# Kernel tuning notes

Hardware: AMD Instinct MI355X
Metric: run time of the kernel (lower is better)

## Reference

```python
import jax, jax.numpy as jnp
import numpy as np

D_MODEL = 1024
N_HEADS = 16
HEAD_DIM = D_MODEL // N_HEADS
BATCH = 2
SEQ = 2048


def setup_inputs() -> dict:
    key = jax.random.key(0)
    ks = jax.random.split(key, 9)
    s = 1.0 / np.sqrt(D_MODEL)
    inp = {
        "x": jax.random.normal(ks[0], (BATCH, SEQ, D_MODEL), dtype=jnp.float32),
        "Wq": jax.random.uniform(ks[1], (D_MODEL, D_MODEL), jnp.float32, -s, s),
        "bq": jax.random.uniform(ks[2], (D_MODEL,), jnp.float32, -s, s),
        "Wk": jax.random.uniform(ks[3], (D_MODEL, D_MODEL), jnp.float32, -s, s),
        "bk": jax.random.uniform(ks[4], (D_MODEL,), jnp.float32, -s, s),
        "Wv": jax.random.uniform(ks[5], (D_MODEL, D_MODEL), jnp.float32, -s, s),
        "bv": jax.random.uniform(ks[6], (D_MODEL,), jnp.float32, -s, s),
        "Wo": jax.random.uniform(ks[7], (D_MODEL, D_MODEL), jnp.float32, -s, s),
        "bo": jax.random.uniform(ks[8], (D_MODEL,), jnp.float32, -s, s),
    }
    return inp


def reference(x, Wq, bq, Wk, bk, Wv, bv, Wo, bo):
    B, S, _ = x.shape
    # projections -> [B, H, S, Dh]
    def proj(W, b):
        y = jnp.einsum('bsd,df->bsf', x, W) + b
        return y.reshape(B, S, N_HEADS, HEAD_DIM).transpose(0, 2, 1, 3)
    q = proj(Wq, bq)
    k = proj(Wk, bk)
    v = proj(Wv, bv)
    scores = jnp.einsum('bhqd,bhkd->bhqk', q, k) / jnp.sqrt(jnp.float32(HEAD_DIM))
    mask = jnp.tril(jnp.ones((S, S), dtype=bool))  # [S, S] causal mask
    scores = jnp.where(mask, scores, -jnp.inf)
    weights = jax.nn.softmax(scores, axis=-1)
    h = jnp.einsum('bhqk,bhkd->bhqd', weights, v)
    h = h.transpose(0, 2, 1, 3).reshape(B, S, N_HEADS * HEAD_DIM)
    return jnp.einsum('bsd,df->bsf', h, Wo) + bo
```

## Files before the change

kernel.cpp:

```cpp
#include <hip/hip_runtime.h>
#include <hip/hip_bf16.h>
#include <cmath>

#define D_MODEL 1024
#define NHEADS 16
#define HDIM 64
#define BATCH 2
#define SEQ 2048
#define MROWS (BATCH*SEQ)
#define KDIM 1024

typedef unsigned short ushort_t;
typedef unsigned int uint32;
typedef __attribute__((ext_vector_type(8))) short short8;
typedef __attribute__((ext_vector_type(4))) short short4b;
typedef __attribute__((ext_vector_type(4))) float floatx4;

#define QSCALE 0.1803368801111204f
#define EXP2F(x) __builtin_amdgcn_exp2f(x)

__device__ __forceinline__ ushort_t f2bf(float x) {
    union { float f; uint32 u; } v; v.f = x;
    uint32 r = v.u + 0x7FFFu + ((v.u >> 16) & 1u);
    return (ushort_t)(r >> 16);
}

__device__ __forceinline__ uint32 pkbf(float a, float b) {
    union { __hip_bfloat162 h2; uint32 u; } v;
    v.h2 = __float22bfloat162_rn(make_float2(a, b));
    return v.u;
}

__device__ __forceinline__ void glds16(const void* g, void* l) {
    __builtin_amdgcn_global_load_lds(
        (const __attribute__((address_space(1))) void*)g,
        (__attribute__((address_space(3))) void*)l, 16, 0, 0);
}

__global__ __launch_bounds__(256)
void cvt_all(const float* __restrict__ x, const float* __restrict__ W0,
             const float* __restrict__ W1, const float* __restrict__ W2,
             const float* __restrict__ W3, ushort_t* __restrict__ xb,
             ushort_t* __restrict__ WtQKV, ushort_t* __restrict__ WtO)
{
    const int z = blockIdx.z;
    if (z == 4) {
        size_t idx = ((size_t)blockIdx.y * 32 + blockIdx.x) * 256 + threadIdx.x;
        #pragma unroll
        for (int l = 0; l < 4; ++l) {
            size_t i = ((size_t)l * 262144 + idx) * 4;
            float4 v = *(const float4*)(x + i);
            uint2 o;
            o.x = pkbf(v.x, v.y);
            o.y = pkbf(v.z, v.w);
            *(uint2*)(xb + i) = o;
        }
        return;
    }
    __shared__ float tl[32][33];
    const float* W = (z == 0) ? W0 : (z == 1) ? W1 : (z == 2) ? W2 : W3;
    ushort_t* out = (z < 3) ? (WtQKV + (size_t)z * D_MODEL * KDIM) : WtO;
    const int k0 = blockIdx.x * 32, n0 = blockIdx.y * 32;
    const int tx = threadIdx.x & 31, ty = threadIdx.x >> 5;
    #pragma unroll
    for (int i = 0; i < 4; ++i)
        tl[ty + i * 8][tx] = W[(size_t)(k0 + ty + i * 8) * D_MODEL + n0 + tx];
    __syncthreads();
    #pragma unroll
    for (int i = 0; i < 4; ++i)
        out[(size_t)(n0 + ty + i * 8) * KDIM + k0 + tx] = f2bf(tl[tx][ty + i * 8]);
}

__global__ __launch_bounds__(128, 2)
void gemm_qkv(const ushort_t* __restrict__ A, const ushort_t* __restrict__ Bt,
              const float* __restrict__ b0, const float* __restrict__ b1,
              const float* __restrict__ b2, ushort_t* __restrict__ Qb,
              ushort_t* __restrict__ Kb, ushort_t* __restrict__ Vb)
{
    __shared__ ushort_t As[128 * 64];
    __shared__ ushort_t Bs[128 * 64];

    const int tid = threadIdx.x;
    const int w = tid >> 6, lane = tid & 63;
    const int quad = lane >> 4, col = lane & 15;
    const int m0 = blockIdx.y * 128, n0 = blockIdx.x * 128;

    floatx4 zero = {0.f, 0.f, 0.f, 0.f};
    floatx4 acc[4][8];
    #pragma unroll
    for (int i = 0; i < 4; ++i)
        #pragma unroll
        for (int j = 0; j < 8; ++j) acc[i][j] = zero;

    #pragma unroll 1
    for (int k0 = 0; k0 < KDIM; k0 += 64) {
        #pragma unroll
        for (int i = 0; i < 8; ++i) {
            int c = i * 128 + tid;
            int row = c >> 3;
            int kc = (c & 7) ^ (row & 7);
            glds16(A  + (size_t)(m0 + row) * KDIM + k0 + kc * 8, As + (i * 128 + w * 64) * 8);
            glds16(Bt + (size_t)(n0 + row) * KDIM + k0 + kc * 8, Bs + (i * 128 + w * 64) * 8);
        }
        __syncthreads();
        #pragma unroll
        for (int ks = 0; ks < 2; ++ks) {
            short8 af[4], bfr[8];
            const int kc = ks * 4 + quad;
            #pragma unroll
            for (int mt = 0; mt < 4; ++mt) {
                int r = w * 64 + mt * 16 + col;
                af[mt] = *(const short8*)(As + ((size_t)r * 8 + (kc ^ (r & 7))) * 8);
            }
            #pragma unroll
            for (int nt = 0; nt < 8; ++nt) {
                int r = nt * 16 + col;
                bfr[nt] = *(const short8*)(Bs + ((size_t)r * 8 + (kc ^ (r & 7))) * 8);
            }
            #pragma unroll
            for (int mt = 0; mt < 4; ++mt)
                #pragma unroll
                for (int nt = 0; nt < 8; ++nt)
                    acc[mt][nt] = __builtin_amdgcn_mfma_f32_16x16x32_bf16(
                        af[mt], bfr[nt], acc[mt][nt], 0, 0, 0);
        }
        __syncthreads();
    }

    const int which = n0 >> 10;
    const float* bp = (which == 0) ? b0 : (which == 1) ? b1 : b2;
    if (which < 2) {
        ushort_t* outp = (which == 0) ? Qb : Kb;
        const float scl = (which == 0) ? QSCALE : 1.0f;
        #pragma unroll
        for (int mt = 0; mt < 4; ++mt)
            #pragma unroll
            for (int nt = 0; nt < 8; ++nt) {
                int nn = (n0 + nt * 16 + col) & 1023;
                float bb = bp[nn];
                int h = nn >> 6, d = nn & 63;
                #pragma unroll
                for (int r = 0; r < 4; ++r) {
                    int m = m0 + w * 64 + mt * 16 + quad * 4 + r;
                    int b = m >> 11, s = m & 2047;
                    outp[((size_t)(b * NHEADS + h) * SEQ + s) * HDIM + d] =
                        f2bf((acc[mt][nt][r] + bb) * scl);
                }
            }
    } else {
        #pragma unroll
        for (int mt = 0; mt < 4; ++mt)
            #pragma unroll
            for (int nt = 0; nt < 8; ++nt) {
                int nn = (n0 + nt * 16 + col) & 1023;
                float bb = bp[nn];
                int h = nn >> 6, d = nn & 63;
                int mb = m0 + w * 64 + mt * 16 + quad * 4;
                int b = mb >> 11, s = mb & 2047;
                uint2 pw;
                pw.x = pkbf(acc[mt][nt][0] + bb, acc[mt][nt][1] + bb);
                pw.y = pkbf(acc[mt][nt][2] + bb, acc[mt][nt][3] + bb);
                *(uint2*)(Vb + ((size_t)(b * NHEADS + h) * HDIM + d) * SEQ + s) = pw;
            }
    }
}

__global__ __launch_bounds__(128, 2)
void gemm_o(const ushort_t* __restrict__ A, const ushort_t* __restrict__ Bt,
            const float* __restrict__ b0, float* __restrict__ Cf)
{
    __shared__ ushort_t As[128 * 64];
    __shared__ ushort_t Bs[64 * 64];

    const int tid = threadIdx.x;
    const int w = tid >> 6, lane = tid & 63;
    const int quad = lane >> 4, col = lane & 15;
    const int m0 = blockIdx.y * 128, n0 = blockIdx.x * 64;

    floatx4 zero = {0.f, 0.f, 0.f, 0.f};
    floatx4 acc[4][4];
    #pragma unroll
    for (int i = 0; i < 4; ++i)
        #pragma unroll
        for (int j = 0; j < 4; ++j) acc[i][j] = zero;

    #pragma unroll 1
    for (int k0 = 0; k0 < KDIM; k0 += 64) {
        #pragma unroll
        for (int i = 0; i < 8; ++i) {
            int c = i * 128 + tid;
            int row = c >> 3;
            int kc = (c & 7) ^ (row & 7);
            glds16(A + (size_t)(m0 + row) * KDIM + k0 + kc * 8, As + (i * 128 + w * 64) * 8);
        }
        #pragma unroll
        for (int i = 0; i < 4; ++i) {
            int c = i * 128 + tid;
            int row = c >> 3;
            int kc = (c & 7) ^ (row & 7);
            glds16(Bt + (size_t)(n0 + row) * KDIM + k0 + kc * 8, Bs + (i * 128 + w * 64) * 8);
        }
        __syncthreads();
        #pragma unroll
        for (int ks = 0; ks < 2; ++ks) {
            short8 af[4], bfr[4];
            const int kc = ks * 4 + quad;
            #pragma unroll
            for (int mt = 0; mt < 4; ++mt) {
                int r = w * 64 + mt * 16 + col;
                af[mt] = *(const short8*)(As + ((size_t)r * 8 + (kc ^ (r & 7))) * 8);
            }
            #pragma unroll
            for (int nt = 0; nt < 4; ++nt) {
                int r = nt * 16 + col;
                bfr[nt] = *(const short8*)(Bs + ((size_t)r * 8 + (kc ^ (r & 7))) * 8);
            }
            #pragma unroll
            for (int mt = 0; mt < 4; ++mt)
                #pragma unroll
                for (int nt = 0; nt < 4; ++nt)
                    acc[mt][nt] = __builtin_amdgcn_mfma_f32_16x16x32_bf16(
                        af[mt], bfr[nt], acc[mt][nt], 0, 0, 0);
        }
        __syncthreads();
    }

    #pragma unroll
    for (int mt = 0; mt < 4; ++mt)
        #pragma unroll
        for (int nt = 0; nt < 4; ++nt) {
            int n = n0 + nt * 16 + col;
            float bb = b0[n];
            #pragma unroll
            for (int r = 0; r < 4; ++r) {
                int m = m0 + w * 64 + mt * 16 + quad * 4 + r;
                Cf[(size_t)m * D_MODEL + n] = acc[mt][nt][r] + bb;
            }
        }
}

__global__ __launch_bounds__(256)
void attn_mfma(const ushort_t* __restrict__ Q, const ushort_t* __restrict__ K,
               const ushort_t* __restrict__ Vt, ushort_t* __restrict__ H)
{
    __shared__ __align__(16) float smemf[16640];
    ushort_t* Qs  = (ushort_t*)smemf;
    ushort_t* Ksm = (ushort_t*)(smemf + 2048);
    ushort_t* Vsm = (ushort_t*)(smemf + 6144);
    float* Ored = smemf;
    float* Lred = smemf + 16384;

    const int tid = threadIdx.x;
    const int w = tid >> 6, lane = tid & 63;
    const int quad = lane >> 4, col = lane & 15;
    const int blk = blockIdx.x;
    const int bh = (blk & 7) * 4 + ((blk >> 3) & 3);
    const int pair = blk >> 5;
    const size_t base = (size_t)bh * SEQ * HDIM;
    const ushort_t* Kb = K + base;
    const ushort_t* Vb = Vt + base;
    const int b = bh >> 4, h = bh & 15;

    const int c0 = (w * 2 + 0) * 64 + lane;
    const int c1 = (w * 2 + 1) * 64 + lane;
    const int r0 = c0 >> 3, o0 = ((c0 & 7) ^ (r0 & 7)) * 8;
    const int r1 = c1 >> 3, o1 = ((c1 & 7) ^ (r1 & 7)) * 8;

    const int rk = w * 16 + col;
    const floatx4 zero = {0.f, 0.f, 0.f, 0.f};

    #pragma unroll 1
    for (int pi = 0; pi < 2; ++pi) {
        const int qt = pi ? pair : 31 - pair;
        const int q0 = qt * 64;
        const int nt = qt + 1;

        __syncthreads();
        #pragma unroll
        for (int i = 0; i < 2; ++i) {
            int c = (w * 2 + i) * 64 + lane;
            int row = c >> 3, kc = (c & 7) ^ (row & 7);
            glds16(Q + base + (size_t)(q0 + row) * HDIM + kc * 8, Qs + (w * 2 + i) * 512);
        }
        glds16(Kb + (size_t)r0 * HDIM + o0, Ksm + (w * 2 + 0) * 512);
        glds16(Kb + (size_t)r1 * HDIM + o1, Ksm + (w * 2 + 1) * 512);
        glds16(Vb + (size_t)r0 * SEQ + o0,  Vsm + (w * 2 + 0) * 512);
        glds16(Vb + (size_t)r1 * SEQ + o1,  Vsm + (w * 2 + 1) * 512);
        __syncthreads();

        short8 bq[4][2];
        #pragma unroll
        for (int qb = 0; qb < 4; ++qb)
            #pragma unroll
            for (int ks = 0; ks < 2; ++ks) {
                int rq = qb * 16 + col;
                int kc = ks * 4 + quad;
                bq[qb][ks] = *(const short8*)(Qs + ((size_t)rq * 8 + (kc ^ (rq & 7))) * 8);
            }

        floatx4 o_[4][4];
        #pragma unroll
        for (int i = 0; i < 4; ++i)
            #pragma unroll
            for (int j = 0; j < 4; ++j) o_[i][j] = zero;
        float lq[4] = {0.f, 0.f, 0.f, 0.f};

        #pragma unroll 1
        for (int t = 0; t < nt; ++t) {
            const ushort_t* Kcur = Ksm + (t & 1) * 4096;
            const ushort_t* Vcur = Vsm + (t & 1) * 4096;
            if (t + 1 < nt) {
                const int k0n = (t + 1) * 64;
                ushort_t* Kn = Ksm + ((t + 1) & 1) * 4096;
                ushort_t* Vn = Vsm + ((t + 1) & 1) * 4096;
                glds16(Kb + (size_t)(k0n + r0) * HDIM + o0, Kn + (w * 2 + 0) * 512);
                glds16(Kb + (size_t)(k0n + r1) * HDIM + o1, Kn + (w * 2 + 1) * 512);
                glds16(Vb + (size_t)r0 * SEQ + k0n + o0,    Vn + (w * 2 + 0) * 512);
                glds16(Vb + (size_t)r1 * SEQ + k0n + o1,    Vn + (w * 2 + 1) * 512);
            }

            floatx4 sc[4];
            #pragma unroll
            for (int qb = 0; qb < 4; ++qb) sc[qb] = zero;
            #pragma unroll
            for (int ks = 0; ks < 2; ++ks) {
                const int kc = ks * 4 + quad;
                short8 ak = *(const short8*)(Kcur + ((size_t)rk * 8 + (kc ^ (rk & 7))) * 8);
                #pragma unroll
                for (int qb = 0; qb < 4; ++qb)
                    sc[qb] = __builtin_amdgcn_mfma_f32_16x16x32_bf16(
                        ak, bq[qb][ks], sc[qb], 0, 0, 0);
            }

            if (t == nt - 1) {
                #pragma unroll
                for (int qb = 0; qb < 4; ++qb)
                    #pragma unroll
                    for (int r = 0; r < 4; ++r)
                        if (w * 16 + quad * 4 + r > qb * 16 + col) sc[qb][r] = -INFINITY;
            }

            short4b bp[4];
            #pragma unroll
            for (int qb = 0; qb < 4; ++qb) {
                float p0 = EXP2F(sc[qb][0]);
                float p1 = EXP2F(sc[qb][1]);
                float p2 = EXP2F(sc[qb][2]);
                float p3 = EXP2F(sc[qb][3]);
                lq[qb] += (p0 + p1) + (p2 + p3);
                union { uint2 u; short4b s; } pv;
                pv.u.x = pkbf(p0, p1);
                pv.u.y = pkbf(p2, p3);
                bp[qb] = pv.s;
            }

            const int cc = 2 * w + (quad >> 1);
            const int sub = (quad & 1) * 4;
            #pragma unroll
            for (int db = 0; db < 4; ++db) {
                int rv = db * 16 + col;
                short4b av = *(const short4b*)(Vcur + ((size_t)rv * 8 + (cc ^ (rv & 7))) * 8 + sub);
                #pragma unroll
                for (int qb = 0; qb < 4; ++qb)
                    o_[db][qb] = __builtin_amdgcn_mfma_f32_16x16x16bf16_1k(
                        av, bp[qb], o_[db][qb], 0, 0, 0);
            }

            __syncthreads();
        }

        #pragma unroll
        for (int qb = 0; qb < 4; ++qb) {
            lq[qb] += __shfl_xor(lq[qb], 16);
            lq[qb] += __shfl_xor(lq[qb], 32);
        }
        if (quad == 0) {
            #pragma unroll
            for (int qb = 0; qb < 4; ++qb) Lred[w * 64 + qb * 16 + col] = lq[qb];
        }
        {
            float* myreg = Ored + w * 4096;
            #pragma unroll
            for (int db = 0; db < 4; ++db)
                #pragma unroll
                for (int qb = 0; qb < 4; ++qb) {
                    int q = qb * 16 + col;
                    int swch = (db * 4 + quad) ^ col;
                    *(floatx4*)(myreg + q * 64 + swch * 4) = o_[db][qb];
                }
        }
        __syncthreads();

        {
            const int qloc = w * 16 + (lane >> 2);
            float lsum = Lred[qloc] + Lred[64 + qloc] + Lred[128 + qloc] + Lred[192 + qloc];
            float linv = 1.f / lsum;
            const int dc0 = (lane & 3) * 4;
            floatx4 acc[4];
            #pragma unroll
            for (int j = 0; j < 4; ++j) {
                int swch = (dc0 + j) ^ (qloc & 15);
                const float* p = Ored + (size_t)qloc * 64 + swch * 4;
                floatx4 a = *(const floatx4*)p;
                a += *(const floatx4*)(p + 4096);
                a += *(const floatx4*)(p + 8192);
                a += *(const floatx4*)(p + 12288);
                acc[j] = a;
            }
            const size_t rowb = ((size_t)(b * SEQ + q0 + qloc)) * D_MODEL + h * HDIM + dc0 * 4;
            uint4 u0, u1;
            u0.x = pkbf(acc[0][0] * linv, acc[0][1] * linv);
            u0.y = pkbf(acc[0][2] * linv, acc[0][3] * linv);
            u0.z = pkbf(acc[1][0] * linv, acc[1][1] * linv);
            u0.w = pkbf(acc[1][2] * linv, acc[1][3] * linv);
            u1.x = pkbf(acc[2][0] * linv, acc[2][1] * linv);
            u1.y = pkbf(acc[2][2] * linv, acc[2][3] * linv);
            u1.z = pkbf(acc[3][0] * linv, acc[3][1] * linv);
            u1.w = pkbf(acc[3][2] * linv, acc[3][3] * linv);
            *(uint4*)(H + rowb) = u0;
            *(uint4*)(H + rowb + 8) = u1;
        }
    }
}

extern "C" void kernel_launch(void* const* d_in, const int* in_sizes, int n_in,
                              void* d_out, int out_size, void* d_ws, size_t ws_size,
                              hipStream_t stream)
{
    (void)in_sizes; (void)n_in; (void)out_size; (void)ws_size;
    const float* x  = (const float*)d_in[0];
    const float* Wq = (const float*)d_in[1];
    const float* bq = (const float*)d_in[2];
    const float* Wk = (const float*)d_in[3];
    const float* bk = (const float*)d_in[4];
    const float* Wv = (const float*)d_in[5];
    const float* bv = (const float*)d_in[6];
    const float* Wo = (const float*)d_in[7];
    const float* bo = (const float*)d_in[8];

    const size_t E = (size_t)MROWS * D_MODEL;
    ushort_t* xb    = (ushort_t*)d_ws;
    ushort_t* WtQKV = xb + E;
    ushort_t* WtO   = WtQKV + 3 * (size_t)D_MODEL * KDIM;
    ushort_t* Qb    = WtO + (size_t)D_MODEL * KDIM;
    ushort_t* Kb    = Qb + E;
    ushort_t* Vb    = Kb + E;
    ushort_t* Hb    = Vb + E;

    cvt_all<<<dim3(32, 32, 5), 256, 0, stream>>>(x, Wq, Wk, Wv, Wo, xb, WtQKV, WtO);
    gemm_qkv<<<dim3(24, 32), 128, 0, stream>>>(xb, WtQKV, bq, bk, bv, Qb, Kb, Vb);
    attn_mfma<<<dim3(512), 256, 0, stream>>>(Qb, Kb, Vb, Hb);
    gemm_o<<<dim3(16, 32), 128, 0, stream>>>(Hb, WtO, bo, (float*)d_out);
}
```

Measured before the change: 179.2 us.

## Fuse conversion, QKV GEMM, attention and output GEMM into one persistent kernel

New measurement: 389.1 us. 2.17x slower.

```diff
diff --git a/kernel.cpp b/kernel.cpp
--- a/kernel.cpp
+++ b/kernel.cpp
@@ -9,6 +9,7 @@
 #define SEQ 2048
 #define MROWS (BATCH*SEQ)
 #define KDIM 1024
+#define NB 512
 
 typedef unsigned short ushort_t;
 typedef unsigned int uint32;
@@ -37,389 +38,432 @@
         (__attribute__((address_space(3))) void*)l, 16, 0, 0);
 }
 
-__global__ __launch_bounds__(256)
-void cvt_all(const float* __restrict__ x, const float* __restrict__ W0,
-             const float* __restrict__ W1, const float* __restrict__ W2,
-             const float* __restrict__ W3, ushort_t* __restrict__ xb,
-             ushort_t* __restrict__ WtQKV, ushort_t* __restrict__ WtO)
+__device__ __forceinline__ void grid_sync(unsigned* bar) {
+    __syncthreads();
+    if (threadIdx.x == 0) {
+        __threadfence();
+        unsigned g = __hip_atomic_load(&bar[1], __ATOMIC_RELAXED, __HIP_MEMORY_SCOPE_AGENT);
+        unsigned old = __hip_atomic_fetch_add(&bar[0], 1u, __ATOMIC_ACQ_REL, __HIP_MEMORY_SCOPE_AGENT);
+        if (old == NB - 1u) {
+            __hip_atomic_store(&bar[0], 0u, __ATOMIC_RELAXED, __HIP_MEMORY_SCOPE_AGENT);
+            __hip_atomic_fetch_add(&bar[1], 1u, __ATOMIC_RELEASE, __HIP_MEMORY_SCOPE_AGENT);
+        } else {
+            while (__hip_atomic_load(&bar[1], __ATOMIC_RELAXED, __HIP_MEMORY_SCOPE_AGENT) == g)
+                __builtin_amdgcn_s_sleep(8);
+        }
+        __threadfence();
+    }
+    __syncthreads();
+}
+
+__global__ void bar_init(unsigned* bar) {
+    if (threadIdx.x < 2) bar[threadIdx.x] = 0u;
+}
+
+__global__ __launch_bounds__(256, 2)
+void mega(const float* __restrict__ x,
+          const float* __restrict__ Wq, const float* __restrict__ bq,
+          const float* __restrict__ Wk, const float* __restrict__ bk,
+          const float* __restrict__ Wv, const float* __restrict__ bv,
+          const float* __restrict__ Wo, const float* __restrict__ bo,
+          ushort_t* __restrict__ xb, ushort_t* __restrict__ WtQKV,
+          ushort_t* __restrict__ WtO, ushort_t* __restrict__ Qb,
+          ushort_t* __restrict__ Kb, ushort_t* __restrict__ Vb,
+          ushort_t* __restrict__ Hb, float* __restrict__ Cf,
+          unsigned* __restrict__ bar)
 {
-    const int z = blockIdx.z;
-    if (z == 4) {
-        size_t idx = ((size_t)blockIdx.y * 32 + blockIdx.x) * 256 + threadIdx.x;
+    __shared__ __align__(16) float smemf[16640];
+
+    const int tid = threadIdx.x;
+    const int blk = blockIdx.x;
+    const int w = tid >> 6, lane = tid & 63;
+    const int quad = lane >> 4, col = lane & 15;
+    const floatx4 zero = {0.f, 0.f, 0.f, 0.f};
+
+    {
+        size_t b0i = (size_t)blk * 8192 + tid * 4;
         #pragma unroll
-        for (int l = 0; l < 4; ++l) {
-            size_t i = ((size_t)l * 262144 + idx) * 4;
+        for (int l = 0; l < 8; ++l) {
+            size_t i = b0i + (size_t)l * 1024;
             float4 v = *(const float4*)(x + i);
             uint2 o;
             o.x = pkbf(v.x, v.y);
             o.y = pkbf(v.z, v.w);
             *(uint2*)(xb + i) = o;
         }
-        return;
-    }
-    __shared__ float tl[32][33];
-    const float* W = (z == 0) ? W0 : (z == 1) ? W1 : (z == 2) ? W2 : W3;
-    ushort_t* out = (z < 3) ? (WtQKV + (size_t)z * D_MODEL * KDIM) : WtO;
-    const int k0 = blockIdx.x * 32, n0 = blockIdx.y * 32;
-    const int tx = threadIdx.x & 31, ty = threadIdx.x >> 5;
-    #pragma unroll
-    for (int i = 0; i < 4; ++i)
-        tl[ty + i * 8][tx] = W[(size_t)(k0 + ty + i * 8) * D_MODEL + n0 + tx];
-    __syncthreads();
-    #pragma unroll
-    for (int i = 0; i < 4; ++i)
-        out[(size_t)(n0 + ty + i * 8) * KDIM + k0 + tx] = f2bf(tl[tx][ty + i * 8]);
-}
-
-__global__ __launch_bounds__(128, 2)
-void gemm_qkv(const ushort_t* __restrict__ A, const ushort_t* __restrict__ Bt,
-              const float* __restrict__ b0, const float* __restrict__ b1,
-              const float* __restrict__ b2, ushort_t* __restrict__ Qb,
-              ushort_t* __restrict__ Kb, ushort_t* __restrict__ Vb)
-{
-    __shared__ ushort_t As[128 * 64];
-    __shared__ ushort_t Bs[128 * 64];
-
-    const int tid = threadIdx.x;
-    const int w = tid >> 6, lane = tid & 63;
-    const int quad = lane >> 4, col = lane & 15;
-    const int m0 = blockIdx.y * 128, n0 = blockIdx.x * 128;
-
-    floatx4 zero = {0.f, 0.f, 0.f, 0.f};
-    floatx4 acc[4][8];
-    #pragma unroll
-    for (int i = 0; i < 4; ++i)
+    }
+    {
+        ushort_t* tl = (ushort_t*)smemf;
+        #pragma unroll 1
+        for (int r = 0; r < 2; ++r) {
+            int tt = blk * 2 + r;
+            int z = tt >> 8, ti = tt & 255;
+            int tk = (ti & 15) * 64, tn = (ti >> 4) * 64;
+            const float* W = (z == 0) ? Wq : (z == 1) ? Wk : (z == 2) ? Wv : Wo;
+            ushort_t* out = (z < 3) ? (WtQKV + (size_t)z * 1048576) : WtO;
+            __syncthreads();
+            #pragma unroll
+            for (int j = 0; j < 4; ++j) {
+                int fid = j * 256 + tid;
+                int kl = fid >> 4, c4 = fid & 15;
+                float4 v = *(const float4*)(W + (size_t)(tk + kl) * 1024 + tn + c4 * 4);
+                ushort4 u;
+                u.x = f2bf(v.x); u.y = f2bf(v.y); u.z = f2bf(v.z); u.w = f2bf(v.w);
+                *(ushort4*)(tl + kl * 68 + c4 * 4) = u;
+            }
+            __syncthreads();
+            #pragma unroll
+            for (int j = 0; j < 4; ++j) {
+                int sid = j * 256 + tid;
+                int nl = sid >> 4, k0 = (sid & 15) * 4;
+                ushort4 u;
+                u.x = tl[(k0 + 0) * 68 + nl];
+                u.y = tl[(k0 + 1) * 68 + nl];
+                u.z = tl[(k0 + 2) * 68 + nl];
+                u.w = tl[(k0 + 3) * 68 + nl];
+                *(ushort4*)(out + (size_t)(tn + nl) * 1024 + tk + k0) = u;
+            }
+        }
+    }
+
+    grid_sync(bar);
+
+    {
+        ushort_t* As = (ushort_t*)smemf;
+        ushort_t* Bs = (ushort_t*)smemf + 8192;
+        const int bm = blk >> 4, bn = blk & 15;
+        const int m0 = bm * 128, n0 = bn * 192;
+        const int wm = w >> 1, wn = w & 1;
+
+        floatx4 acc[4][6];
         #pragma unroll
-        for (int j = 0; j < 8; ++j) acc[i][j] = zero;
-
-    #pragma unroll 1
-    for (int k0 = 0; k0 < KDIM; k0 += 64) {
-        #pragma unroll
-        for (int i = 0; i < 8; ++i) {
-            int c = i * 128 + tid;
-            int row = c >> 3;
-            int kc = (c & 7) ^ (row & 7);
-            glds16(A  + (size_t)(m0 + row) * KDIM + k0 + kc * 8, As + (i * 128 + w * 64) * 8);
-            glds16(Bt + (size_t)(n0 + row) * KDIM + k0 + kc * 8, Bs + (i * 128 + w * 64) * 8);
-        }
-        __syncthreads();
-        #pragma unroll
-        for (int ks = 0; ks < 2; ++ks) {
-            short8 af[4], bfr[8];
-            const int kc = ks * 4 + quad;
-            #pragma unroll
-            for (int mt = 0; mt < 4; ++mt) {
-                int r = w * 64 + mt * 16 + col;
-                af[mt] = *(const short8*)(As + ((size_t)r * 8 + (kc ^ (r & 7))) * 8);
-            }
-            #pragma unroll
-            for (int nt = 0; nt < 8; ++nt) {
-                int r = nt * 16 + col;
-                bfr[nt] = *(const short8*)(Bs + ((size_t)r * 8 + (kc ^ (r & 7))) * 8);
-            }
-            #pragma unroll
-            for (int mt = 0; mt < 4; ++mt)
-                #pragma unroll
-                for (int nt = 0; nt < 8; ++nt)
-                    acc[mt][nt] = __builtin_amdgcn_mfma_f32_16x16x32_bf16(
-                        af[mt], bfr[nt], acc[mt][nt], 0, 0, 0);
-        }
-        __syncthreads();
-    }
-
-    const int which = n0 >> 10;
-    const float* bp = (which == 0) ? b0 : (which == 1) ? b1 : b2;
-    if (which < 2) {
-        ushort_t* outp = (which == 0) ? Qb : Kb;
-        const float scl = (which == 0) ? QSCALE : 1.0f;
+        for (int i = 0; i < 4; ++i)
+            #pragma unroll
+            for (int j = 0; j < 6; ++j) acc[i][j] = zero;
+
+        #pragma unroll 1
+        for (int k0 = 0; k0 < KDIM; k0 += 64) {
+            #pragma unroll
+            for (int i = 0; i < 4; ++i) {
+                int c = i * 256 + tid;
+                int row = c >> 3;
+                int kc = (c & 7) ^ (row & 7);
+                glds16(xb + (size_t)(m0 + row) * KDIM + k0 + kc * 8, As + (i * 256 + w * 64) * 8);
+            }
+            #pragma unroll
+            for (int i = 0; i < 6; ++i) {
+                int c = i * 256 + tid;
+                int row = c >> 3;
+                int kc = (c & 7) ^ (row & 7);
+                glds16(WtQKV + (size_t)(n0 + row) * KDIM + k0 + kc * 8, Bs + (i * 256 + w * 64) * 8);
+            }
+            __syncthreads();
+            #pragma unroll
+            for (int ks = 0; ks < 2; ++ks) {
+                short8 af[4], bfr[6];
+                const int kc = ks * 4 + quad;
+                #pragma unroll
+                for (int mt = 0; mt < 4; ++mt) {
+                    int r = wm * 64 + mt * 16 + col;
+                    af[mt] = *(const short8*)(As + ((size_t)r * 8 + (kc ^ (r & 7))) * 8);
+                }
+                #pragma unroll
+                for (int nt = 0; nt < 6; ++nt) {
+                    int r = wn * 96 + nt * 16 + col;
+                    bfr[nt] = *(const short8*)(Bs + ((size_t)r * 8 + (kc ^ (r & 7))) * 8);
+                }
+                #pragma unroll
+                for (int mt = 0; mt < 4; ++mt)
+                    #pragma unroll
+                    for (int nt = 0; nt < 6; ++nt)
+                        acc[mt][nt] = __builtin_amdgcn_mfma_f32_16x16x32_bf16(
+                            af[mt], bfr[nt], acc[mt][nt], 0, 0, 0);
+            }
+            __syncthreads();
+        }
+
         #pragma unroll
         for (int mt = 0; mt < 4; ++mt)
             #pragma unroll
-            for (int nt = 0; nt < 8; ++nt) {
-                int nn = (n0 + nt * 16 + col) & 1023;
-                float bb = bp[nn];
+            for (int nt = 0; nt < 6; ++nt) {
+                int nbase = n0 + wn * 96 + nt * 16;
+                int which = nbase >> 10;
+                int nn = (nbase & 1023) + col;
                 int h = nn >> 6, d = nn & 63;
+                if (which == 0) {
+                    float bb = bq[nn];
+                    #pragma unroll
+                    for (int r = 0; r < 4; ++r) {
+                        int m = m0 + wm * 64 + mt * 16 + quad * 4 + r;
+                        int b = m >> 11, s = m & 2047;
+                        Qb[((size_t)(b * NHEADS + h) * SEQ + s) * HDIM + d] =
+                            f2bf((acc[mt][nt][r] + bb) * QSCALE);
+                    }
+                } else if (which == 1) {
+                    float bb = bk[nn];
+                    #pragma unroll
+                    for (int r = 0; r < 4; ++r) {
+                        int m = m0 + wm * 64 + mt * 16 + quad * 4 + r;
+                        int b = m >> 11, s = m & 2047;
+                        Kb[((size_t)(b * NHEADS + h) * SEQ + s) * HDIM + d] =
+                            f2bf(acc[mt][nt][r] + bb);
+                    }
+                } else {
+                    float bb = bv[nn];
+                    int mb = m0 + wm * 64 + mt * 16 + quad * 4;
+                    int b = mb >> 11, s = mb & 2047;
+                    uint2 pw;
+                    pw.x = pkbf(acc[mt][nt][0] + bb, acc[mt][nt][1] + bb);
+                    pw.y = pkbf(acc[mt][nt][2] + bb, acc[mt][nt][3] + bb);
+                    *(uint2*)(Vb + ((size_t)(b * NHEADS + h) * HDIM + d) * SEQ + s) = pw;
+                }
+            }
+    }
+
+    grid_sync(bar);
+
+    {
+        ushort_t* Qs  = (ushort_t*)smemf;
+        ushort_t* Ksm = (ushort_t*)(smemf + 2048);
+        ushort_t* Vsm = (ushort_t*)(smemf + 6144);
+        float* Ored = smemf;
+        float* Lred = smemf + 16384;
+
+        const int bh = (blk & 7) * 4 + ((blk >> 3) & 3);
+        const int pair = blk >> 5;
+        const size_t base = (size_t)bh * SEQ * HDIM;
+        const ushort_t* Kp = Kb + base;
+        const ushort_t* Vp = Vb + base;
+        const int bi = bh >> 4, hi = bh & 15;
+
+        const int c0 = (w * 2 + 0) * 64 + lane;
+        const int c1 = (w * 2 + 1) * 64 + lane;
+        const int r0 = c0 >> 3, o0 = ((c0 & 7) ^ (r0 & 7)) * 8;
+        const int r1 = c1 >> 3, o1 = ((c1 & 7) ^ (r1 & 7)) * 8;
+
+        const int rk = w * 16 + col;
+
+        #pragma unroll 1
+        for (int pi = 0; pi < 2; ++pi) {
+            const int qt = pi ? pair : 31 - pair;
+            const int q0 = qt * 64;
+            const int ntk = qt + 1;
+
+            __syncthreads();
+            #pragma unroll
+            for (int i = 0; i < 2; ++i) {
+                int c = (w * 2 + i) * 64 + lane;
+                int row = c >> 3, kc = (c & 7) ^ (row & 7);
+                glds16(Qb + base + (size_t)(q0 + row) * HDIM + kc * 8, Qs + (w * 2 + i) * 512);
+            }
+            glds16(Kp + (size_t)r0 * HDIM + o0, Ksm + (w * 2 + 0) * 512);
+            glds16(Kp + (size_t)r1 * HDIM + o1, Ksm + (w * 2 + 1) * 512);
+            glds16(Vp + (size_t)r0 * SEQ + o0,  Vsm + (w * 2 + 0) * 512);
+            glds16(Vp + (size_t)r1 * SEQ + o1,  Vsm + (w * 2 + 1) * 512);
+            __syncthreads();
+
+            short8 qf[4][2];
+            #pragma unroll
+            for (int qb2 = 0; qb2 < 4; ++qb2)
+                #pragma unroll
+                for (int ks = 0; ks < 2; ++ks) {
+                    int rq = qb2 * 16 + col;
+                    int kc = ks * 4 + quad;
+                    qf[qb2][ks] = *(const short8*)(Qs + ((size_t)rq * 8 + (kc ^ (rq & 7))) * 8);
+                }
+
+            floatx4 o_[4][4];
+            #pragma unroll
+            for (int i = 0; i < 4; ++i)
+                #pragma unroll
+                for (int j = 0; j < 4; ++j) o_[i][j] = zero;
+            float lq[4] = {0.f, 0.f, 0.f, 0.f};
+
+            #pragma unroll 1
+            for (int t = 0; t < ntk; ++t) {
+                const ushort_t* Kcur = Ksm + (t & 1) * 4096;
+                const ushort_t* Vcur = Vsm + (t & 1) * 4096;
+                if (t + 1 < ntk) {
+                    const int k0n = (t + 1) * 64;
+                    ushort_t* Kn = Ksm + ((t + 1) & 1) * 4096;
+                    ushort_t* Vn = Vsm + ((t + 1) & 1) * 4096;
+                    glds16(Kp + (size_t)(k0n + r0) * HDIM + o0, Kn + (w * 2 + 0) * 512);
+                    glds16(Kp + (size_t)(k0n + r1) * HDIM + o1, Kn + (w * 2 + 1) * 512);
+                    glds16(Vp + (size_t)r0 * SEQ + k0n + o0,    Vn + (w * 2 + 0) * 512);
+                    glds16(Vp + (size_t)r1 * SEQ + k0n + o1,    Vn + (w * 2 + 1) * 512);
+                }
+
+                floatx4 sc[4];
+                #pragma unroll
+                for (int qb2 = 0; qb2 < 4; ++qb2) sc[qb2] = zero;
+                #pragma unroll
+                for (int ks = 0; ks < 2; ++ks) {
+                    const int kc = ks * 4 + quad;
+                    short8 ak = *(const short8*)(Kcur + ((size_t)rk * 8 + (kc ^ (rk & 7))) * 8);
+                    #pragma unroll
+                    for (int qb2 = 0; qb2 < 4; ++qb2)
+                        sc[qb2] = __builtin_amdgcn_mfma_f32_16x16x32_bf16(
+                            ak, qf[qb2][ks], sc[qb2], 0, 0, 0);
+                }
+
+                if (t == ntk - 1) {
+                    #pragma unroll
+                    for (int qb2 = 0; qb2 < 4; ++qb2)
+                        #pragma unroll
+                        for (int r = 0; r < 4; ++r)
+                            if (w * 16 + quad * 4 + r > qb2 * 16 + col) sc[qb2][r] = -INFINITY;
+                }
+
+                short4b bp[4];
+                #pragma unroll
+                for (int qb2 = 0; qb2 < 4; ++qb2) {
+                    float p0 = EXP2F(sc[qb2][0]);
+                    float p1 = EXP2F(sc[qb2][1]);
+                    float p2 = EXP2F(sc[qb2][2]);
+                    float p3 = EXP2F(sc[qb2][3]);
+                    lq[qb2] += (p0 + p1) + (p2 + p3);
+                    union { uint2 u; short4b s; } pv;
+                    pv.u.x = pkbf(p0, p1);
+                    pv.u.y = pkbf(p2, p3);
+                    bp[qb2] = pv.s;
+                }
+
+                const int cc = 2 * w + (quad >> 1);
+                const int sub = (quad & 1) * 4;
+                #pragma unroll
+                for (int db = 0; db < 4; ++db) {
+                    int rv = db * 16 + col;
+                    short4b av = *(const short4b*)(Vcur + ((size_t)rv * 8 + (cc ^ (rv & 7))) * 8 + sub);
+                    #pragma unroll
+                    for (int qb2 = 0; qb2 < 4; ++qb2)
+                        o_[db][qb2] = __builtin_amdgcn_mfma_f32_16x16x16bf16_1k(
+                            av, bp[qb2], o_[db][qb2], 0, 0, 0);
+                }
+
+                __syncthreads();
+            }
+
+            #pragma unroll
+            for (int qb2 = 0; qb2 < 4; ++qb2) {
+                lq[qb2] += __shfl_xor(lq[qb2], 16);
+                lq[qb2] += __shfl_xor(lq[qb2], 32);
+            }
+            if (quad == 0) {
+                #pragma unroll
+                for (int qb2 = 0; qb2 < 4; ++qb2) Lred[w * 64 + qb2 * 16 + col] = lq[qb2];
+            }
+            {
+                float* myreg = Ored + w * 4096;
+                #pragma unroll
+                for (int db = 0; db < 4; ++db)
+                    #pragma unroll
+                    for (int qb2 = 0; qb2 < 4; ++qb2) {
+                        int q = qb2 * 16 + col;
+                        int swch = (db * 4 + quad) ^ col;
+                        *(floatx4*)(myreg + q * 64 + swch * 4) = o_[db][qb2];
+                    }
+            }
+            __syncthreads();
+
+            {
+                const int qloc = w * 16 + (lane >> 2);
+                float lsum = Lred[qloc] + Lred[64 + qloc] + Lred[128 + qloc] + Lred[192 + qloc];
+                float linv = 1.f / lsum;
+                const int dc0 = (lane & 3) * 4;
+                floatx4 accv[4];
+                #pragma unroll
+                for (int j = 0; j < 4; ++j) {
+                    int swch = (dc0 + j) ^ (qloc & 15);
+                    const float* p = Ored + (size_t)qloc * 64 + swch * 4;
+                    floatx4 a = *(const floatx4*)p;
+                    a += *(const floatx4*)(p + 4096);
+                    a += *(const floatx4*)(p + 8192);
+                    a += *(const floatx4*)(p + 12288);
+                    accv[j] = a;
+                }
+                const size_t rowb = ((size_t)(bi * SEQ + q0 + qloc)) * D_MODEL + hi * HDIM + dc0 * 4;
+                uint4 u0, u1;
+                u0.x = pkbf(accv[0][0] * linv, accv[0][1] * linv);
+                u0.y = pkbf(accv[0][2] * linv, accv[0][3] * linv);
+                u0.z = pkbf(accv[1][0] * linv, accv[1][1] * linv);
+                u0.w = pkbf(accv[1][2] * linv, accv[1][3] * linv);
+                u1.x = pkbf(accv[2][0] * linv, accv[2][1] * linv);
+                u1.y = pkbf(accv[2][2] * linv, accv[2][3] * linv);
+                u1.z = pkbf(accv[3][0] * linv, accv[3][1] * linv);
+                u1.w = pkbf(accv[3][2] * linv, accv[3][3] * linv);
+                *(uint4*)(Hb + rowb) = u0;
+                *(uint4*)(Hb + rowb + 8) = u1;
+            }
+        }
+    }
+
+    grid_sync(bar);
+
+    {
+        ushort_t* As = (ushort_t*)smemf;
+        ushort_t* Bs = (ushort_t*)smemf + 8192;
+        const int bm = blk >> 4, bn = blk & 15;
+        const int m0 = bm * 128, n0 = bn * 64;
+
+        floatx4 acc[2][4];
+        #pragma unroll
+        for (int i = 0; i < 2; ++i)
+            #pragma unroll
+            for (int j = 0; j < 4; ++j) acc[i][j] = zero;
+
+        #pragma unroll 1
+        for (int k0 = 0; k0 < KDIM; k0 += 64) {
+            #pragma unroll
+            for (int i = 0; i < 4; ++i) {
+                int c = i * 256 + tid;
+                int row = c >> 3;
+                int kc = (c & 7) ^ (row & 7);
+                glds16(Hb + (size_t)(m0 + row) * KDIM + k0 + kc * 8, As + (i * 256 + w * 64) * 8);
+            }
+            #pragma unroll
+            for (int i = 0; i < 2; ++i) {
+                int c = i * 256 + tid;
+                int row = c >> 3;
+                int kc = (c & 7) ^ (row & 7);
+                glds16(WtO + (size_t)(n0 + row) * KDIM + k0 + kc * 8, Bs + (i * 256 + w * 64) * 8);
+            }
+            __syncthreads();
+            #pragma unroll
+            for (int ks = 0; ks < 2; ++ks) {
+                short8 af[2], bfr[4];
+                const int kc = ks * 4 + quad;
+                #pragma unroll
+                for (int mt = 0; mt < 2; ++mt) {
+                    int r = w * 32 + mt * 16 + col;
+                    af[mt] = *(const short8*)(As + ((size_t)r * 8 + (kc ^ (r & 7))) * 8);
+                }
+                #pragma unroll
+                for (int nt = 0; nt < 4; ++nt) {
+                    int r = nt * 16 + col;
+                    bfr[nt] = *(const short8*)(Bs + ((size_t)r * 8 + (kc ^ (r & 7))) * 8);
+                }
+                #pragma unroll
+                for (int mt = 0; mt < 2; ++mt)
+                    #pragma unroll
+                    for (int nt = 0; nt < 4; ++nt)
+                        acc[mt][nt] = __builtin_amdgcn_mfma_f32_16x16x32_bf16(
+                            af[mt], bfr[nt], acc[mt][nt], 0, 0, 0);
+            }
+            __syncthreads();
+        }
+
+        #pragma unroll
+        for (int mt = 0; mt < 2; ++mt)
+            #pragma unroll
+            for (int nt = 0; nt < 4; ++nt) {
+                int n = n0 + nt * 16 + col;
+                float bb = bo[n];
                 #pragma unroll
                 for (int r = 0; r < 4; ++r) {
-                    int m = m0 + w * 64 + mt * 16 + quad * 4 + r;
-                    int b = m >> 11, s = m & 2047;
-                    outp[((size_t)(b * NHEADS + h) * SEQ + s) * HDIM + d] =
-                        f2bf((acc[mt][nt][r] + bb) * scl);
-                }
-            }
-    } else {
-        #pragma unroll
-        for (int mt = 0; mt < 4; ++mt)
-            #pragma unroll
-            for (int nt = 0; nt < 8; ++nt) {
-                int nn = (n0 + nt * 16 + col) & 1023;
-                float bb = bp[nn];
-                int h = nn >> 6, d = nn & 63;
-                int mb = m0 + w * 64 + mt * 16 + quad * 4;
-                int b = mb >> 11, s = mb & 2047;
-                uint2 pw;
-                pw.x = pkbf(acc[mt][nt][0] + bb, acc[mt][nt][1] + bb);
-                pw.y = pkbf(acc[mt][nt][2] + bb, acc[mt][nt][3] + bb);
-                *(uint2*)(Vb + ((size_t)(b * NHEADS + h) * HDIM + d) * SEQ + s) = pw;
-            }
-    }
-}
-
-__global__ __launch_bounds__(128, 2)
-void gemm_o(const ushort_t* __restrict__ A, const ushort_t* __restrict__ Bt,
-            const float* __restrict__ b0, float* __restrict__ Cf)
-{
-    __shared__ ushort_t As[128 * 64];
-    __shared__ ushort_t Bs[64 * 64];
-
-    const int tid = threadIdx.x;
-    const int w = tid >> 6, lane = tid & 63;
-    const int quad = lane >> 4, col = lane & 15;
-    const int m0 = blockIdx.y * 128, n0 = blockIdx.x * 64;
-
-    floatx4 zero = {0.f, 0.f, 0.f, 0.f};
-    floatx4 acc[4][4];
-    #pragma unroll
-    for (int i = 0; i < 4; ++i)
-        #pragma unroll
-        for (int j = 0; j < 4; ++j) acc[i][j] = zero;
-
-    #pragma unroll 1
-    for (int k0 = 0; k0 < KDIM; k0 += 64) {
-        #pragma unroll
-        for (int i = 0; i < 8; ++i) {
-            int c = i * 128 + tid;
-            int row = c >> 3;
-            int kc = (c & 7) ^ (row & 7);
-            glds16(A + (size_t)(m0 + row) * KDIM + k0 + kc * 8, As + (i * 128 + w * 64) * 8);
-        }
-        #pragma unroll
-        for (int i = 0; i < 4; ++i) {
-            int c = i * 128 + tid;
-            int row = c >> 3;
-            int kc = (c & 7) ^ (row & 7);
-            glds16(Bt + (size_t)(n0 + row) * KDIM + k0 + kc * 8, Bs + (i * 128 + w * 64) * 8);
-        }
-        __syncthreads();
-        #pragma unroll
-        for (int ks = 0; ks < 2; ++ks) {
-            short8 af[4], bfr[4];
-            const int kc = ks * 4 + quad;
-            #pragma unroll
-            for (int mt = 0; mt < 4; ++mt) {
-                int r = w * 64 + mt * 16 + col;
-                af[mt] = *(const short8*)(As + ((size_t)r * 8 + (kc ^ (r & 7))) * 8);
-            }
-            #pragma unroll
-            for (int nt = 0; nt < 4; ++nt) {
-                int r = nt * 16 + col;
-                bfr[nt] = *(const short8*)(Bs + ((size_t)r * 8 + (kc ^ (r & 7))) * 8);
-            }
-            #pragma unroll
-            for (int mt = 0; mt < 4; ++mt)
-                #pragma unroll
-                for (int nt = 0; nt < 4; ++nt)
-                    acc[mt][nt] = __builtin_amdgcn_mfma_f32_16x16x32_bf16(
-                        af[mt], bfr[nt], acc[mt][nt], 0, 0, 0);
-        }
-        __syncthreads();
-    }
-
-    #pragma unroll
-    for (int mt = 0; mt < 4; ++mt)
-        #pragma unroll
-        for (int nt = 0; nt < 4; ++nt) {
-            int n = n0 + nt * 16 + col;
-            float bb = b0[n];
-            #pragma unroll
-            for (int r = 0; r < 4; ++r) {
-                int m = m0 + w * 64 + mt * 16 + quad * 4 + r;
-                Cf[(size_t)m * D_MODEL + n] = acc[mt][nt][r] + bb;
-            }
-        }
-}
-
-__global__ __launch_bounds__(256)
-void attn_mfma(const ushort_t* __restrict__ Q, const ushort_t* __restrict__ K,
-               const ushort_t* __restrict__ Vt, ushort_t* __restrict__ H)
-{
-    __shared__ __align__(16) float smemf[16640];
-    ushort_t* Qs  = (ushort_t*)smemf;
-    ushort_t* Ksm = (ushort_t*)(smemf + 2048);
-    ushort_t* Vsm = (ushort_t*)(smemf + 6144);
-    float* Ored = smemf;
-    float* Lred = smemf + 16384;
-
-    const int tid = threadIdx.x;
-    const int w = tid >> 6, lane = tid & 63;
-    const int quad = lane >> 4, col = lane & 15;
-    const int blk = blockIdx.x;
-    const int bh = (blk & 7) * 4 + ((blk >> 3) & 3);
-    const int pair = blk >> 5;
-    const size_t base = (size_t)bh * SEQ * HDIM;
-    const ushort_t* Kb = K + base;
-    const ushort_t* Vb = Vt + base;
-    const int b = bh >> 4, h = bh & 15;
-
-    const int c0 = (w * 2 + 0) * 64 + lane;
-    const int c1 = (w * 2 + 1) * 64 + lane;
-    const int r0 = c0 >> 3, o0 = ((c0 & 7) ^ (r0 & 7)) * 8;
-    const int r1 = c1 >> 3, o1 = ((c1 & 7) ^ (r1 & 7)) * 8;
-
-    const int rk = w * 16 + col;
-    const floatx4 zero = {0.f, 0.f, 0.f, 0.f};
-
-    #pragma unroll 1
-    for (int pi = 0; pi < 2; ++pi) {
-        const int qt = pi ? pair : 31 - pair;
-        const int q0 = qt * 64;
-        const int nt = qt + 1;
-
-        __syncthreads();
-        #pragma unroll
-        for (int i = 0; i < 2; ++i) {
-            int c = (w * 2 + i) * 64 + lane;
-            int row = c >> 3, kc = (c & 7) ^ (row & 7);
-            glds16(Q + base + (size_t)(q0 + row) * HDIM + kc * 8, Qs + (w * 2 + i) * 512);
-        }
-        glds16(Kb + (size_t)r0 * HDIM + o0, Ksm + (w * 2 + 0) * 512);
-        glds16(Kb + (size_t)r1 * HDIM + o1, Ksm + (w * 2 + 1) * 512);
-        glds16(Vb + (size_t)r0 * SEQ + o0,  Vsm + (w * 2 + 0) * 512);
-        glds16(Vb + (size_t)r1 * SEQ + o1,  Vsm + (w * 2 + 1) * 512);
-        __syncthreads();
-
-        short8 bq[4][2];
-        #pragma unroll
-        for (int qb = 0; qb < 4; ++qb)
-            #pragma unroll
-            for (int ks = 0; ks < 2; ++ks) {
-                int rq = qb * 16 + col;
-                int kc = ks * 4 + quad;
-                bq[qb][ks] = *(const short8*)(Qs + ((size_t)rq * 8 + (kc ^ (rq & 7))) * 8);
-            }
-
-        floatx4 o_[4][4];
-        #pragma unroll
-        for (int i = 0; i < 4; ++i)
-            #pragma unroll
-            for (int j = 0; j < 4; ++j) o_[i][j] = zero;
-        float lq[4] = {0.f, 0.f, 0.f, 0.f};
-
-        #pragma unroll 1
-        for (int t = 0; t < nt; ++t) {
-            const ushort_t* Kcur = Ksm + (t & 1) * 4096;
-            const ushort_t* Vcur = Vsm + (t & 1) * 4096;
-            if (t + 1 < nt) {
-                const int k0n = (t + 1) * 64;
-                ushort_t* Kn = Ksm + ((t + 1) & 1) * 4096;
-                ushort_t* Vn = Vsm + ((t + 1) & 1) * 4096;
-                glds16(Kb + (size_t)(k0n + r0) * HDIM + o0, Kn + (w * 2 + 0) * 512);
-                glds16(Kb + (size_t)(k0n + r1) * HDIM + o1, Kn + (w * 2 + 1) * 512);
-                glds16(Vb + (size_t)r0 * SEQ + k0n + o0,    Vn + (w * 2 + 0) * 512);
-                glds16(Vb + (size_t)r1 * SEQ + k0n + o1,    Vn + (w * 2 + 1) * 512);
-            }
-
-            floatx4 sc[4];
-            #pragma unroll
-            for (int qb = 0; qb < 4; ++qb) sc[qb] = zero;
-            #pragma unroll
-            for (int ks = 0; ks < 2; ++ks) {
-                const int kc = ks * 4 + quad;
-                short8 ak = *(const short8*)(Kcur + ((size_t)rk * 8 + (kc ^ (rk & 7))) * 8);
-                #pragma unroll
-                for (int qb = 0; qb < 4; ++qb)
-                    sc[qb] = __builtin_amdgcn_mfma_f32_16x16x32_bf16(
-                        ak, bq[qb][ks], sc[qb], 0, 0, 0);
-            }
-
-            if (t == nt - 1) {
-                #pragma unroll
-                for (int qb = 0; qb < 4; ++qb)
-                    #pragma unroll
-                    for (int r = 0; r < 4; ++r)
-                        if (w * 16 + quad * 4 + r > qb * 16 + col) sc[qb][r] = -INFINITY;
-            }
-
-            short4b bp[4];
-            #pragma unroll
-            for (int qb = 0; qb < 4; ++qb) {
-                float p0 = EXP2F(sc[qb][0]);
-                float p1 = EXP2F(sc[qb][1]);
-                float p2 = EXP2F(sc[qb][2]);
-                float p3 = EXP2F(sc[qb][3]);
-                lq[qb] += (p0 + p1) + (p2 + p3);
-                union { uint2 u; short4b s; } pv;
-                pv.u.x = pkbf(p0, p1);
-                pv.u.y = pkbf(p2, p3);
-                bp[qb] = pv.s;
-            }
-
-            const int cc = 2 * w + (quad >> 1);
-            const int sub = (quad & 1) * 4;
-            #pragma unroll
-            for (int db = 0; db < 4; ++db) {
-                int rv = db * 16 + col;
-                short4b av = *(const short4b*)(Vcur + ((size_t)rv * 8 + (cc ^ (rv & 7))) * 8 + sub);
-                #pragma unroll
-                for (int qb = 0; qb < 4; ++qb)
-                    o_[db][qb] = __builtin_amdgcn_mfma_f32_16x16x16bf16_1k(
-                        av, bp[qb], o_[db][qb], 0, 0, 0);
-            }
-
-            __syncthreads();
-        }
-
-        #pragma unroll
-        for (int qb = 0; qb < 4; ++qb) {
-            lq[qb] += __shfl_xor(lq[qb], 16);
-            lq[qb] += __shfl_xor(lq[qb], 32);
-        }
-        if (quad == 0) {
-            #pragma unroll
-            for (int qb = 0; qb < 4; ++qb) Lred[w * 64 + qb * 16 + col] = lq[qb];
-        }
-        {
-            float* myreg = Ored + w * 4096;
-            #pragma unroll
-            for (int db = 0; db < 4; ++db)
-                #pragma unroll
-                for (int qb = 0; qb < 4; ++qb) {
-                    int q = qb * 16 + col;
-                    int swch = (db * 4 + quad) ^ col;
-                    *(floatx4*)(myreg + q * 64 + swch * 4) = o_[db][qb];
-                }
-        }
-        __syncthreads();
-
-        {
-            const int qloc = w * 16 + (lane >> 2);
-            float lsum = Lred[qloc] + Lred[64 + qloc] + Lred[128 + qloc] + Lred[192 + qloc];
-            float linv = 1.f / lsum;
-            const int dc0 = (lane & 3) * 4;
-            floatx4 acc[4];
-            #pragma unroll
-            for (int j = 0; j < 4; ++j) {
-                int swch = (dc0 + j) ^ (qloc & 15);
-                const float* p = Ored + (size_t)qloc * 64 + swch * 4;
-                floatx4 a = *(const floatx4*)p;
-                a += *(const floatx4*)(p + 4096);
-                a += *(const floatx4*)(p + 8192);
-                a += *(const floatx4*)(p + 12288);
-                acc[j] = a;
-            }
-            const size_t rowb = ((size_t)(b * SEQ + q0 + qloc)) * D_MODEL + h * HDIM + dc0 * 4;
-            uint4 u0, u1;
-            u0.x = pkbf(acc[0][0] * linv, acc[0][1] * linv);
-            u0.y = pkbf(acc[0][2] * linv, acc[0][3] * linv);
-            u0.z = pkbf(acc[1][0] * linv, acc[1][1] * linv);
-            u0.w = pkbf(acc[1][2] * linv, acc[1][3] * linv);
-            u1.x = pkbf(acc[2][0] * linv, acc[2][1] * linv);
-            u1.y = pkbf(acc[2][2] * linv, acc[2][3] * linv);
-            u1.z = pkbf(acc[3][0] * linv, acc[3][1] * linv);
-            u1.w = pkbf(acc[3][2] * linv, acc[3][3] * linv);
-            *(uint4*)(H + rowb) = u0;
-            *(uint4*)(H + rowb + 8) = u1;
-        }
+                    int m = m0 + w * 32 + mt * 16 + quad * 4 + r;
+                    Cf[(size_t)m * D_MODEL + n] = acc[mt][nt][r] + bb;
+                }
+            }
     }
 }
 
@@ -446,9 +490,10 @@
     ushort_t* Kb    = Qb + E;
     ushort_t* Vb    = Kb + E;
     ushort_t* Hb    = Vb + E;
-
-    cvt_all<<<dim3(32, 32, 5), 256, 0, stream>>>(x, Wq, Wk, Wv, Wo, xb, WtQKV, WtO);
-    gemm_qkv<<<dim3(24, 32), 128, 0, stream>>>(xb, WtQKV, bq, bk, bv, Qb, Kb, Vb);
-    attn_mfma<<<dim3(512), 256, 0, stream>>>(Qb, Kb, Vb, Hb);
-    gemm_o<<<dim3(16, 32), 128, 0, stream>>>(Hb, WtO, bo, (float*)d_out);
-}
+    unsigned* bar   = (unsigned*)(Hb + E);
+
+    bar_init<<<1, 64, 0, stream>>>(bar);
+    mega<<<dim3(NB), 256, 0, stream>>>(x, Wq, bq, Wk, bk, Wv, bv, Wo, bo,
+                                       xb, WtQKV, WtO, Qb, Kb, Vb, Hb,
+                                       (float*)d_out, bar);
+}
```
